# Kernel tuning notes

Measured on AMD Instinct MI355X. Metric: run time of the kernel, lower is better.

## Reference

```python
import jax, jax.numpy as jnp
import numpy as np
import math

B, S, D, NS, K, V = 4, 1024, 256, 64, 16, 32000
NEG = -10000.0


def l2n(x, axis=-1):
    # F.normalize with eps=1e-12
    return x / jnp.maximum(jnp.linalg.norm(x, axis=axis, keepdims=True), 1e-12)


def sparsemax(z, axis=-1):
    # sort descending, find support size k_z, threshold tau
    z_sorted = -jnp.sort(-z, axis=axis)
    cumsum = jnp.cumsum(z_sorted, axis=axis)
    n = z.shape[axis]
    k = jnp.arange(1, n + 1, dtype=z.dtype).reshape((1,) * (z.ndim - 1) + (n,))
    check = (1.0 + k * z_sorted > cumsum).astype(z.dtype)
    k_z = jnp.sum(check, axis=axis, keepdims=True)
    tau = (jnp.take_along_axis(cumsum, (k_z - 1).astype(jnp.int32), axis=axis) - 1.0) / k_z
    return jnp.maximum(z - tau, 0.0)


def router_forward(messages, hidden, x_ids, scn, mask, static_nb, geo_velocity,
                   ctx_conf, current_entropy, vel_proj_w, edge_w1, edge_b1,
                   edge_w2, edge_b2, probe_w, geo_gate_w, geo_gate_b):
    S_ = messages.shape[1]
    dg = jnp.eye(S_, dtype=bool)
    mfull = mask[None] | dg[None]  # masked_fill(mask) + diagonal fill combined

    # --- geodesic-endpoint routed attention ---
    endpoint = l2n(scn + 0.4 * geo_velocity)                      # [B,S,NS]
    endpoint_sim = jnp.einsum('bsn,btn->bst', endpoint, scn)      # [B,S,S]
    endpoint_sim = jnp.where(mfull, NEG, endpoint_sim)
    H_norm = jax.lax.stop_gradient(current_entropy)[..., None] / (math.log(V) + 1e-8)
    vel_h = geo_velocity @ vel_proj_w.T                           # [B,S,D]
    h_aimed = l2n(hidden + 0.3 * vel_h)
    h_msg_sim = jnp.einsum('bsd,btd->bst', h_aimed, messages)
    combined_geo = (endpoint_sim * H_norm + 0.5 * h_msg_sim) * 5.0
    combined_geo = jnp.where(mfull, NEG, combined_geo)
    ew_geo = sparsemax(combined_geo, axis=-1)
    geo_agg = jnp.einsum('bst,btd->bsd', ew_geo, messages)

    # --- vocab-neighbor match / aggregate ---
    nb_vocab = static_nb[x_ids]                                   # [B,S,K]
    match = (x_ids[:, None, None, :] == nb_vocab[..., None]).astype(messages.dtype)  # [B,S,K,S]
    causal = jnp.tril(jnp.ones((S_, S_), messages.dtype))
    match = match * causal[None, :, None, :]
    coverage = jnp.mean(jnp.minimum(jnp.sum(match, -1), 1.0), axis=-1, keepdims=True)  # [B,S,1]
    nb_msgs_s = jnp.einsum('bskp,bpd->bskd', match, messages)
    nb_scn_s = jnp.einsum('bskp,bpn->bskn', match, scn)
    sim_s = jnp.sum(nb_scn_s * scn[:, :, None, :], -1)            # [B,S,K]
    e = jax.nn.gelu(sim_s[..., None] @ edge_w1.T + edge_b1, approximate=False)
    e = (e @ edge_w2.T + edge_b2)[..., 0]
    ew_s = jax.nn.softmax(e, axis=-1)
    static_agg = jnp.sum(nb_msgs_s * ew_s[..., None], axis=2)     # [B,S,D]

    # --- local same-mode routing with sparsemax ---
    my_mode = jnp.argmax(scn, -1)
    same_mode = (my_mode[:, :, None] == my_mode[:, None, :]).astype(messages.dtype)
    same_mode = jnp.where(mfull, 0.0, same_mode)
    scn_sim = jnp.einsum('bsn,btn->bst', scn, scn) * same_mode
    has_nb = jnp.sum(same_mode, -1, keepdims=True) > 0
    pos = jnp.arange(S_, dtype=messages.dtype)
    pos_sim = -jnp.abs(pos[:, None] - pos[None, :])[None]
    pos_sim = jnp.where(mfull, NEG, pos_sim)
    routing_sim = jnp.where(has_nb, scn_sim, pos_sim * 0.01)
    routing_sim = jnp.where(mfull, NEG, routing_sim)
    ew_l = sparsemax(routing_sim * 5.0, axis=-1)
    local_agg = jnp.einsum('bst,btd->bsd', ew_l, messages)

    static_final = coverage * static_agg + (1.0 - coverage) * local_agg
    raw_gate = jax.nn.sigmoid(hidden @ geo_gate_w.T + geo_gate_b)
    geo_weight = raw_gate * ctx_conf
    agg = geo_weight * geo_agg + (1.0 - geo_weight) * static_final
    probe = l2n(hidden @ probe_w.T)
    agg_n = l2n(agg)
    rel = jax.nn.sigmoid(jnp.sum(agg_n * probe, -1, keepdims=True))
    return agg * rel


def setup_inputs() -> dict:
    key = jax.random.key(0)
    ks = jax.random.split(key, 14)
    messages = jax.random.normal(ks[0], (B, S, D), jnp.float32)
    hidden = jax.random.normal(ks[1], (B, S, D), jnp.float32)
    x_ids = jax.random.randint(ks[2], (B, S), 0, V)
    scn = jax.random.normal(ks[3], (B, S, NS), jnp.float32)
    mask = ~jnp.tril(jnp.ones((S, S), bool))  # True above diagonal (disallowed)
    static_nb = jax.random.randint(ks[4], (V, K), 0, V)
    geo_velocity = jax.random.normal(ks[5], (B, S, NS), jnp.float32) * 0.5
    ctx_conf = jax.random.uniform(ks[6], (B, S, 1), jnp.float32)
    current_entropy = jax.random.uniform(ks[7], (B, S), jnp.float32) * math.log(V)
    vel_proj_w = jax.random.normal(ks[8], (D, NS), jnp.float32) / np.sqrt(NS).astype(np.float32)
    edge_w1 = jax.random.normal(ks[9], (8, 1), jnp.float32)
    edge_b1 = jnp.zeros((8,), jnp.float32)
    edge_w2 = jax.random.normal(ks[10], (1, 8), jnp.float32) * 0.3
    edge_b2 = jnp.zeros((1,), jnp.float32)
    probe_w = jax.random.normal(ks[11], (D, D), jnp.float32) / np.sqrt(D).astype(np.float32)
    geo_gate_w = jax.random.normal(ks[12], (1, D), jnp.float32) * 0.02
    geo_gate_b = jnp.full((1,), -4.0, jnp.float32)
    return dict(messages=messages, hidden=hidden, x_ids=x_ids, scn=scn, mask=mask,
                static_nb=static_nb, geo_velocity=geo_velocity, ctx_conf=ctx_conf,
                current_entropy=current_entropy, vel_proj_w=vel_proj_w,
                edge_w1=edge_w1, edge_b1=edge_b1, edge_w2=edge_w2, edge_b2=edge_b2,
                probe_w=probe_w, geo_gate_w=geo_gate_w, geo_gate_b=geo_gate_b)


def reference(messages, hidden, x_ids, scn, mask, static_nb, geo_velocity, ctx_conf,
              current_entropy, vel_proj_w, edge_w1, edge_b1, edge_w2, edge_b2,
              probe_w, geo_gate_w, geo_gate_b):
    return router_forward(messages, hidden, x_ids, scn, mask, static_nb, geo_velocity,
                          ctx_conf, current_entropy, vel_proj_w, edge_w1, edge_b1,
                          edge_w2, edge_b2, probe_w, geo_gate_w, geo_gate_b)
```

## Files before the change

kernel.cpp:

```cpp
#include <hip/hip_runtime.h>
#include <math.h>

#define B_ 4
#define S_ 1024
#define D_ 256
#define NS_ 64
#define KNB 16
#define KPACK 320
#define NEG_ (-10000.0f)
#define LOGV_INV (1.0f/(10.373491181781864f + 1e-8f))
#define MCAP 64
#define NCHUNK 16
#define SUPCAP 1024

typedef __attribute__((ext_vector_type(8))) short short8;
typedef __attribute__((ext_vector_type(4))) float f32x4;


__device__ __forceinline__ void blockReduceSum4(float4& v, float* red) {
  #pragma unroll
  for (int off = 32; off > 0; off >>= 1) {
    v.x += __shfl_down(v.x, off, 64);
    v.y += __shfl_down(v.y, off, 64);
    v.z += __shfl_down(v.z, off, 64);
    v.w += __shfl_down(v.w, off, 64);
  }
  int lane = threadIdx.x & 63;
  int w = threadIdx.x >> 6;
  __syncthreads();
  if (lane == 0) {
    red[w] = v.x; red[4 + w] = v.y; red[8 + w] = v.z; red[12 + w] = v.w;
  }
  __syncthreads();
  v.x = red[0] + red[1] + red[2] + red[3];
  v.y = red[4] + red[5] + red[6] + red[7];
  v.z = red[8] + red[9] + red[10] + red[11];
  v.w = red[12] + red[13] + red[14] + red[15];
}

__device__ __forceinline__ void waveAllSum2(float& a, float& b) {
  #pragma unroll
  for (int off = 1; off < 64; off <<= 1) {
    a += __shfl_xor(a, off, 64);
    b += __shfl_xor(b, off, 64);
  }
}

__device__ __forceinline__ float michelot_tau16(const float* z) {
  float m = z[0];
  #pragma unroll
  for (int k = 1; k < 16; k++) m = fmaxf(m, z[k]);
  #pragma unroll
  for (int off = 1; off < 64; off <<= 1) m = fmaxf(m, __shfl_xor(m, off, 64));
  float thr = m - 1.0f;
  float s = 0.f, c = 0.f;
  #pragma unroll
  for (int k = 0; k < 16; k++) { float zk = z[k]; if (zk > thr) { s += zk; c += 1.f; } }
  waveAllSum2(s, c);
  int cnt = (int)c;
  float tau = (s - 1.0f) / c;
  for (int it = 0; it < 32; ++it) {
    float s2 = 0.f, c2 = 0.f;
    #pragma unroll
    for (int k = 0; k < 16; k++) { float zk = z[k]; if (zk > tau) { s2 += zk; c2 += 1.f; } }
    waveAllSum2(s2, c2);
    int ci = (int)c2;
    if (ci == cnt || ci == 0) break;
    cnt = ci;
    tau = (s2 - 1.0f) / c2;
  }
  return tau;
}

__device__ __forceinline__ unsigned short f2bf_rne(float f) {
  union { float f; unsigned u; } v; v.f = f;
  unsigned r = v.u + 0x7FFFu + ((v.u >> 16) & 1u);
  return (unsigned short)(r >> 16);
}
__device__ __forceinline__ float bf2f(unsigned short h) {
  union { unsigned u; float f; } v; v.u = ((unsigned)h) << 16;
  return v.f;
}
__device__ __forceinline__ void cvt_store4(unsigned short* hi, unsigned short* lo, float4 v) {
  unsigned short h0 = f2bf_rne(v.x), h1 = f2bf_rne(v.y), h2 = f2bf_rne(v.z), h3 = f2bf_rne(v.w);
  *(ushort4*)hi = make_ushort4(h0, h1, h2, h3);
  *(ushort4*)lo = make_ushort4(f2bf_rne(v.x - bf2f(h0)), f2bf_rne(v.y - bf2f(h1)),
                               f2bf_rne(v.z - bf2f(h2)), f2bf_rne(v.w - bf2f(h3)));
}
#define MFMA16(a,b,c) __builtin_amdgcn_mfma_f32_16x16x32_bf16((a),(b),(c),0,0,0)


__global__ __launch_bounds__(256) void msum_partial_kernel(
    const float* __restrict__ messages, float* __restrict__ part)
{
  int blk = blockIdx.x;
  int b = blk >> 4, c = blk & 15;
  int d = threadIdx.x;
  const float* src = messages + ((size_t)b * S_ + c * 64) * D_ + d;
  float acc = 0.f;
  #pragma unroll 8
  for (int t = 0; t < 64; t++) acc += src[t * D_];
  part[((size_t)b * NCHUNK + c) * D_ + d] = acc;
}


__global__ __launch_bounds__(256) void dual_gemm_kernel(
    const float* __restrict__ hidden, const float* __restrict__ gv,
    const float* __restrict__ probe_w, const float* __restrict__ vel_w,
    float* __restrict__ probe_raw, float* __restrict__ vel_h)
{
  __shared__ float As[32][68];
  __shared__ float Bs[32][68];
  int which = blockIdx.y;
  const float* A = which ? gv : hidden;
  const float* W = which ? vel_w : probe_w;
  float* C = which ? vel_h : probe_raw;
  int K = which ? NS_ : D_;

  int mt = blockIdx.x >> 2;
  int nt = blockIdx.x & 3;
  int s0 = mt * 64, t0 = nt * 64;

  int tid = threadIdx.x;
  int tx = tid & 15, ty = tid >> 4;
  float acc[4][4] = {{0.f}};

  for (int k0 = 0; k0 < K; k0 += 32) {
    #pragma unroll
    for (int l = 0; l < 2; l++) {
      int idx = tid + l * 256;
      int i = idx >> 3;
      int kf = idx & 7;
      float4 av = *(const float4*)(A + (size_t)(s0 + i) * K + k0 + kf*4);
      As[kf*4+0][i] = av.x; As[kf*4+1][i] = av.y; As[kf*4+2][i] = av.z; As[kf*4+3][i] = av.w;
      float4 bv = *(const float4*)(W + (size_t)(t0 + i) * K + k0 + kf*4);
      Bs[kf*4+0][i] = bv.x; Bs[kf*4+1][i] = bv.y; Bs[kf*4+2][i] = bv.z; Bs[kf*4+3][i] = bv.w;
    }
    __syncthreads();
    #pragma unroll
    for (int kk = 0; kk < 32; kk++) {
      float4 a4 = *(const float4*)&As[kk][ty*4];
      float4 b4 = *(const float4*)&Bs[kk][tx*4];
      float a[4] = {a4.x, a4.y, a4.z, a4.w};
      float bb[4] = {b4.x, b4.y, b4.z, b4.w};
      #pragma unroll
      for (int rr = 0; rr < 4; rr++)
        #pragma unroll
        for (int cc = 0; cc < 4; cc++)
          acc[rr][cc] += a[rr] * bb[cc];
    }
    __syncthreads();
  }

  #pragma unroll
  for (int rr = 0; rr < 4; rr++) {
    int srow = s0 + ty*4 + rr;
    float4 v = make_float4(acc[rr][0], acc[rr][1], acc[rr][2], acc[rr][3]);
    *(float4*)(C + (size_t)srow * D_ + t0 + tx*4) = v;
  }
}


__global__ __launch_bounds__(256) void prep2_kernel(
    const float* __restrict__ hidden,
    const float* __restrict__ scn, const float* __restrict__ gv,
    const float* __restrict__ ctx_conf, const float* __restrict__ entropy,
    const float* __restrict__ probe_raw, const float* __restrict__ vel_h,
    const float* __restrict__ gate_w, const float* __restrict__ gate_b,
    float* __restrict__ arow,
    float* __restrict__ probe, float* __restrict__ gw_out,
    int* __restrict__ mode_out)
{
  int r = blockIdx.x;
  int tid = threadIdx.x;
  __shared__ float sh_scn[NS_];
  __shared__ float red[16];

  float sv = 0.f, gvv = 0.f;
  if (tid < NS_) {
    sv  = scn[(size_t)r*NS_ + tid];
    gvv = gv[(size_t)r*NS_ + tid];
    sh_scn[tid] = sv;
  }
  float hid = hidden[(size_t)r*D_ + tid];
  float vh  = vel_h[(size_t)r*D_ + tid];
  float pr  = probe_raw[(size_t)r*D_ + tid];
  float gwt = gate_w[tid];

  float ep = (tid < NS_) ? (sv + 0.4f*gvv) : 0.f;
  float ha = hid + 0.3f*vh;

  float4 v = make_float4(ep*ep, ha*ha, pr*pr, hid*gwt);
  blockReduceSum4(v, red);

  float Hn = entropy[r] * LOGV_INV;
  float epn = fmaxf(sqrtf(v.x), 1e-12f);
  float han = fmaxf(sqrtf(v.y), 1e-12f);
  float prn = fmaxf(sqrtf(v.z), 1e-12f);

  if (tid < NS_) {
    arow[(size_t)r*KPACK + tid] = (5.0f*Hn) * (ep / epn);
  }
  arow[(size_t)r*KPACK + NS_ + tid] = 2.5f * (ha / han);
  probe[(size_t)r*D_ + tid] = pr / prn;

  if (tid == 0) {
    float rg = 1.f/(1.f + expf(-(v.w + gate_b[0])));
    gw_out[r] = rg * ctx_conf[r];
    float m = sh_scn[0]; int mi = 0;
    for (int n = 1; n < NS_; n++) { if (sh_scn[n] > m) { m = sh_scn[n]; mi = n; } }
    mode_out[r] = mi;
  }
}


#define GBT 64
#define GBK 32
#define NTRI 136
#define LDB 40

__global__ __launch_bounds__(256) void geo_gemm_mfma_kernel(
    const float* __restrict__ arow, const float* __restrict__ scn,
    const float* __restrict__ messages, float* __restrict__ z,
    float* __restrict__ sim)
{
  __shared__ unsigned short Ahi[GBT][LDB], Alo[GBT][LDB];
  __shared__ unsigned short Bhi[GBT][LDB], Blo[GBT][LDB];
  __shared__ unsigned short A2hi[GBT][LDB], A2lo[GBT][LDB];

  int blk = blockIdx.x;
  int b = blk / NTRI;
  int tri = blk % NTRI;
  int ts = 0;
  while ((ts + 1) * (ts + 2) / 2 <= tri) ts++;
  int tt = tri - ts * (ts + 1) / 2;
  int s0 = ts * GBT, t0 = tt * GBT;

  const float* A  = arow + (size_t)b * S_ * KPACK;
  const float* Bscn = scn + (size_t)b * S_ * NS_;
  const float* Bmsg = messages + (size_t)b * S_ * D_;

  int tid = threadIdx.x;
  int lane = tid & 63;
  int w = tid >> 6;
  int fm = lane & 15;
  int fq = lane >> 4;

  f32x4 accz[4], accs[4];
  #pragma unroll
  for (int i = 0; i < 4; i++) {
    accz[i] = (f32x4){0.f, 0.f, 0.f, 0.f};
    accs[i] = (f32x4){0.f, 0.f, 0.f, 0.f};
  }

  for (int k0 = 0; k0 < KPACK; k0 += GBK) {
    bool scn_slab = (k0 < NS_);
    #pragma unroll
    for (int l = 0; l < 2; l++) {
      int idx = tid + l * 256;
      int i = idx >> 3, kf = idx & 7;
      float4 av = *(const float4*)(A + (size_t)(s0 + i) * KPACK + k0 + kf*4);
      cvt_store4(&Ahi[i][kf*4], &Alo[i][kf*4], av);
      float4 bv;
      if (scn_slab) bv = *(const float4*)(Bscn + (size_t)(t0 + i) * NS_ + k0 + kf*4);
      else          bv = *(const float4*)(Bmsg + (size_t)(t0 + i) * D_ + (k0 - NS_) + kf*4);
      cvt_store4(&Bhi[i][kf*4], &Blo[i][kf*4], bv);
      if (scn_slab) {
        float4 cv = *(const float4*)(Bscn + (size_t)(s0 + i) * NS_ + k0 + kf*4);
        cvt_store4(&A2hi[i][kf*4], &A2lo[i][kf*4], cv);
      }
    }
    __syncthreads();

    short8 ah = *(const short8*)&Ahi[w*16 + fm][fq*8];
    short8 al = *(const short8*)&Alo[w*16 + fm][fq*8];
    short8 a2h, a2l;
    if (scn_slab) {
      a2h = *(const short8*)&A2hi[w*16 + fm][fq*8];
      a2l = *(const short8*)&A2lo[w*16 + fm][fq*8];
    }
    #pragma unroll
    for (int nt = 0; nt < 4; nt++) {
      short8 bh = *(const short8*)&Bhi[nt*16 + fm][fq*8];
      short8 bl = *(const short8*)&Blo[nt*16 + fm][fq*8];
      accz[nt] = MFMA16(ah, bh, accz[nt]);
      accz[nt] = MFMA16(ah, bl, accz[nt]);
      accz[nt] = MFMA16(al, bh, accz[nt]);
      if (scn_slab) {
        accs[nt] = MFMA16(a2h, bh, accs[nt]);
        accs[nt] = MFMA16(a2h, bl, accs[nt]);
        accs[nt] = MFMA16(a2l, bh, accs[nt]);
      }
    }
    __syncthreads();
  }

  float* zb = z + (size_t)b * S_ * S_;
  float* sb = sim + (size_t)b * S_ * S_;
  #pragma unroll
  for (int nt = 0; nt < 4; nt++) {
    #pragma unroll
    for (int rg = 0; rg < 4; rg++) {
      int row = s0 + w*16 + fq*4 + rg;
      int col = t0 + nt*16 + fm;
      zb[(size_t)row * S_ + col] = accz[nt][rg];
      sb[(size_t)row * S_ + col] = accs[nt][rg];
    }
  }
}


__global__ __launch_bounds__(256) void rows_fused7_kernel(
    const float* __restrict__ zbuf, const float* __restrict__ simbuf,
    const float* __restrict__ messages, const int* __restrict__ mode,
    const int* __restrict__ x_ids, const int* __restrict__ static_nb,
    const float* __restrict__ ew1, const float* __restrict__ eb1,
    const float* __restrict__ ew2, const float* __restrict__ eb2,
    const float* __restrict__ gw, const float* __restrict__ probe,
    const float* __restrict__ part, float* __restrict__ out)
{
  __shared__ int xb_l[S_];
  __shared__ int mode_l[S_];
  __shared__ float sim_lds[2][S_];
  __shared__ unsigned short gt_l[2][SUPCAP];
  __shared__ float gw_l[2][SUPCAP];
  __shared__ unsigned short lt_l[2][SUPCAP];
  __shared__ float lw_l[2][SUPCAP];
  __shared__ int gcnt_s[2], lcnt_s[2];
  __shared__ unsigned short mk_s[2][MCAP];
  __shared__ unsigned short mp_s[2][MCAP];
  __shared__ float ews[2][KNB];
  __shared__ float cov_s[2];
  __shared__ int M_s[2];
  __shared__ float red2[2][2][2];

  const int tid = threadIdx.x;
  const int lane = tid & 63;
  const int wv = tid >> 6;
  const int rw = wv >> 1;
  const int half = wv & 1;
  const int r = blockIdx.x * 2 + rw;
  const int b = r >> 10, s = r & 1023;
  const unsigned long long lmask_lt = (1ull << lane) - 1ull;

  const float2* msg2 = (const float2*)(messages + (size_t)b * S_ * D_);
  const int dbase = half * 64 + lane;

  ((int4*)xb_l)[tid]   = ((const int4*)(x_ids + (size_t)b * S_))[tid];
  ((int4*)mode_l)[tid] = ((const int4*)(mode + (size_t)b * S_))[tid];
  {
    int wr = tid & 127;
    const float4* simrow4 = (const float4*)(simbuf + (size_t)r * S_);
    if (wr * 4 <= s)         ((float4*)sim_lds[rw])[wr]       = simrow4[wr];
    if ((wr + 128) * 4 <= s) ((float4*)sim_lds[rw])[wr + 128] = simrow4[wr + 128];
  }
  __syncthreads();

  if (half == 0) {
    if (s != 0) {
      const float4* zrow4 = (const float4*)(zbuf + (size_t)r * S_);
      float zg[16];
      #pragma unroll
      for (int j = 0; j < 4; j++) {
        int t0 = j*256 + lane*4;
        if (j*256 < s) {
          float4 v = zrow4[j*64 + lane];
          zg[j*4+0] = (t0+0 < s) ? v.x : NEG_;
          zg[j*4+1] = (t0+1 < s) ? v.y : NEG_;
          zg[j*4+2] = (t0+2 < s) ? v.z : NEG_;
          zg[j*4+3] = (t0+3 < s) ? v.w : NEG_;
        } else {
          zg[j*4+0] = NEG_; zg[j*4+1] = NEG_; zg[j*4+2] = NEG_; zg[j*4+3] = NEG_;
        }
      }
      float tau = michelot_tau16(zg);
      int base = 0;
      #pragma unroll
      for (int k = 0; k < 16; k++) {
        float w = zg[k] - tau;
        bool p = w > 0.f;
        unsigned long long m = __ballot(p);
        if (p) {
          int idx = base + __popcll(m & lmask_lt);
          gt_l[rw][idx] = (unsigned short)((k >> 2)*256 + lane*4 + (k & 3));
          gw_l[rw][idx] = w;
        }
        base += __popcll(m);
      }
      if (lane == 0) gcnt_s[rw] = base;
    } else if (lane == 0) gcnt_s[rw] = 0;

    int xid = xb_l[s];
    int nb[KNB];
    #pragma unroll
    for (int k = 0; k < KNB; k++) nb[k] = static_nb[(size_t)xid * KNB + k];
    float simk[KNB];
    #pragma unroll
    for (int k = 0; k < KNB; k++) simk[k] = 0.f;
    unsigned int kmask = 0;
    int M = 0;
    for (int j = 0; j < 16; j++) {
      int p = j*64 + lane;
      int xp = xb_l[p];
      bool anym = false;
      #pragma unroll
      for (int k = 0; k < KNB; k++) anym |= (nb[k] == xp);
      anym = anym && (p <= s);
      unsigned long long m = __ballot(anym);
      while (m) {
        int ln = __ffsll((unsigned long long)m) - 1; m &= m - 1;
        int pp = j*64 + ln;
        int xpp = xb_l[pp];
        float d = sim_lds[rw][pp];
        #pragma unroll
        for (int k = 0; k < KNB; k++) {
          if (nb[k] == xpp) {
            if (M < MCAP && lane == 0) { mk_s[rw][M] = (unsigned short)k; mp_s[rw][M] = (unsigned short)pp; }
            M++;
            simk[k] += d;
            kmask |= (1u << k);
          }
        }
      }
    }
    if (M > MCAP) M = MCAP;
    if (lane == 0) { M_s[rw] = M; cov_s[rw] = (float)__popc(kmask) * (1.0f/(float)KNB); }
    if (M > 0) {
      if (lane == 0) {
        #pragma unroll
        for (int k = 0; k < KNB; k++) ews[rw][k] = simk[k];
      }
      float sim = (lane < KNB) ? ews[rw][lane] : 0.f;
      float e = eb2[0];
      #pragma unroll
      for (int j = 0; j < 8; j++) {
        float x = sim * ew1[j] + eb1[j];
        float gx = 0.5f * x * (1.0f + erff(x * 0.70710678118654752f));
        e += gx * ew2[j];
      }
      float mx = e;
      #pragma unroll
      for (int off = 1; off < 16; off <<= 1) mx = fmaxf(mx, __shfl_xor(mx, off, 64));
      float ex = expf(e - mx);
      float ssum = ex;
      #pragma unroll
      for (int off = 1; off < 16; off <<= 1) ssum += __shfl_xor(ssum, off, 64);
      if (lane < KNB) ews[rw][lane] = ex / ssum;
    }
  } else {
    if (s != 0) {
      int mode_s = mode_l[s];
      int cnt = 0;
      unsigned int pmask = 0;
      #pragma unroll
      for (int j = 0; j < 16; j++) {
        int t = j*64 + lane;
        bool p = (t < s) && (mode_l[t] == mode_s);
        if (p) pmask |= (1u << j);
        cnt += __popcll(__ballot(p));
      }
      bool has_nb = cnt > 0;
      float zl[16];
      #pragma unroll
      for (int j = 0; j < 16; j++) {
        int t = j*64 + lane;
        float zv;
        if (t >= s) zv = NEG_ * 5.0f;
        else if (pmask & (1u << j)) zv = sim_lds[rw][t] * 5.0f;
        else if (has_nb) zv = 0.f;
        else zv = (0.01f * (-(float)(s - t))) * 5.0f;
        zl[j] = zv;
      }
      float tau = michelot_tau16(zl);
      int base = 0;
      #pragma unroll
      for (int j = 0; j < 16; j++) {
        float w = zl[j] - tau;
        bool p = w > 0.f;
        unsigned long long m = __ballot(p);
        if (p) {
          int idx = base + __popcll(m & lmask_lt);
          lt_l[rw][idx] = (unsigned short)(j*64 + lane);
          lw_l[rw][idx] = w;
        }
        base += __popcll(m);
      }
      if (lane == 0) lcnt_s[rw] = base;
    } else if (lane == 0) lcnt_s[rw] = 0;
  }
  __syncthreads();

  float2 accg = {0.f, 0.f}, accl = {0.f, 0.f}, accs = {0.f, 0.f};
  if (s == 0) {
    const float2* part2 = (const float2*)(part + (size_t)b * NCHUNK * D_);
    float2 msum = {0.f, 0.f};
    #pragma unroll
    for (int c = 0; c < NCHUNK; c++) {
      float2 pm = part2[c * 128 + dbase];
      msum.x += pm.x; msum.y += pm.y;
    }
    accg.x = 0.0009765625f * msum.x; accg.y = 0.0009765625f * msum.y;
    accl.x = 0.00390625f * msum.x;   accl.y = 0.00390625f * msum.y;
  } else {
    int gc = gcnt_s[rw];
    for (int i = 0; i < gc; i++) {
      float w = gw_l[rw][i];
      float2 mm = msg2[(size_t)gt_l[rw][i] * 128 + dbase];
      accg.x += w*mm.x; accg.y += w*mm.y;
    }
    int lc = lcnt_s[rw];
    for (int i = 0; i < lc; i++) {
      float w = lw_l[rw][i];
      float2 mm = msg2[(size_t)lt_l[rw][i] * 128 + dbase];
      accl.x += w*mm.x; accl.y += w*mm.y;
    }
  }
  {
    int M = M_s[rw];
    for (int i = 0; i < M; i++) {
      int k = mk_s[rw][i], p = mp_s[rw][i];
      float w = ews[rw][k];
      float2 mm = msg2[(size_t)p * 128 + dbase];
      accs.x += w*mm.x; accs.y += w*mm.y;
    }
  }

  float g = gw[r];
  float cov = cov_s[rw];
  float2 agg;
  agg.x = g*accg.x + (1.f-g)*(cov*accs.x + (1.f-cov)*accl.x);
  agg.y = g*accg.y + (1.f-g)*(cov*accs.y + (1.f-cov)*accl.y);

  float2 pv = ((const float2*)probe)[(size_t)r * 128 + dbase];
  float n2 = agg.x*agg.x + agg.y*agg.y;
  float ap = agg.x*pv.x + agg.y*pv.y;
  waveAllSum2(n2, ap);
  if (lane == 0) { red2[rw][half][0] = n2; red2[rw][half][1] = ap; }
  __syncthreads();
  n2 = red2[rw][0][0] + red2[rw][1][0];
  ap = red2[rw][0][1] + red2[rw][1][1];
  float nrm = fmaxf(sqrtf(n2), 1e-12f);
  float rel = 1.f / (1.f + expf(-(ap / nrm)));
  float2 o;
  o.x = agg.x * rel; o.y = agg.y * rel;
  ((float2*)out)[(size_t)r * 128 + dbase] = o;
}


extern "C" void kernel_launch(void* const* d_in, const int* in_sizes, int n_in,
                              void* d_out, int out_size, void* d_ws, size_t ws_size,
                              hipStream_t stream)
{
  const float* messages  = (const float*)d_in[0];
  const float* hidden    = (const float*)d_in[1];
  const int*   x_ids     = (const int*)d_in[2];
  const float* scn       = (const float*)d_in[3];
  const int*   static_nb = (const int*)d_in[5];
  const float* gv        = (const float*)d_in[6];
  const float* ctx_conf  = (const float*)d_in[7];
  const float* entropy   = (const float*)d_in[8];
  const float* vel_w     = (const float*)d_in[9];
  const float* ew1       = (const float*)d_in[10];
  const float* eb1       = (const float*)d_in[11];
  const float* ew2       = (const float*)d_in[12];
  const float* eb2       = (const float*)d_in[13];
  const float* probe_w   = (const float*)d_in[14];
  const float* gate_w    = (const float*)d_in[15];
  const float* gate_b    = (const float*)d_in[16];
  float* out = (float*)d_out;

  float* ws      = (float*)d_ws;
  float* arow    = ws;
  float* probe   = arow    + (size_t)B_*S_*KPACK;
  float* gwbuf   = probe   + (size_t)B_*S_*D_;
  int*   mode    = (int*)(gwbuf + (size_t)B_*S_);
  float* zbuf    = (float*)(mode + (size_t)B_*S_);
  float* simbuf  = zbuf + (size_t)B_*S_*S_;
  float* vel_h   = simbuf + (size_t)B_*S_*S_;
  float* part    = vel_h + (size_t)B_*S_*D_;

  msum_partial_kernel<<<dim3(B_*NCHUNK), dim3(256), 0, stream>>>(messages, part);

  dual_gemm_kernel<<<dim3(256, 2), dim3(256), 0, stream>>>(
      hidden, gv, probe_w, vel_w, probe, vel_h);

  prep2_kernel<<<dim3(B_*S_), dim3(256), 0, stream>>>(
      hidden, scn, gv, ctx_conf, entropy, probe, vel_h,
      gate_w, gate_b, arow, probe, gwbuf, mode);

  geo_gemm_mfma_kernel<<<dim3(B_*NTRI), dim3(256), 0, stream>>>(
      arow, scn, messages, zbuf, simbuf);

  rows_fused7_kernel<<<dim3(B_*S_/2), dim3(256), 0, stream>>>(
      zbuf, simbuf, messages, mode, x_ids, static_nb,
      ew1, eb1, ew2, eb2, gwbuf, probe, part, out);
}
```

Baseline: 188.5 us.

## Pre-split inputs to bf16 hi/lo, use MFMA for dual GEMM, drop sim LDS staging

Adds a kernel that converts messages, hidden, scn, velocity and the weight matrices into bf16 hi/lo pairs once. The two small projection GEMMs then run on MFMA with a 3-term split instead of scalar FP32, and the geo GEMM loads pre-split bf16 tiles instead of converting inside every tile. The rows kernel stops staging the sim row in LDS and reads simbuf directly, using a shuffle for the match loop. This adds an extra pass and extra workspace traffic, and the hidden/gv splits alias zbuf before it is written.

```diff
diff --git a/kernel.cpp b/kernel.cpp
--- a/kernel.cpp
+++ b/kernel.cpp
@@ -14,6 +14,7 @@
 #define SUPCAP 1024
 
 typedef __attribute__((ext_vector_type(8))) short short8;
+typedef __attribute__((ext_vector_type(8))) unsigned short ushort8v;
 typedef __attribute__((ext_vector_type(4))) float f32x4;
 
 
@@ -88,6 +89,33 @@
                                f2bf_rne(v.z - bf2f(h2)), f2bf_rne(v.w - bf2f(h3)));
 }
 #define MFMA16(a,b,c) __builtin_amdgcn_mfma_f32_16x16x32_bf16((a),(b),(c),0,0,0)
+
+
+__global__ __launch_bounds__(256) void bf16_split_kernel(
+    const float* __restrict__ messages, const float* __restrict__ hidden,
+    const float* __restrict__ scn, const float* __restrict__ gv,
+    const float* __restrict__ probe_w, const float* __restrict__ vel_w,
+    unsigned short* __restrict__ msg_hi, unsigned short* __restrict__ msg_lo,
+    unsigned short* __restrict__ hid_hi, unsigned short* __restrict__ hid_lo,
+    unsigned short* __restrict__ scn_hi, unsigned short* __restrict__ scn_lo,
+    unsigned short* __restrict__ gv_hi,  unsigned short* __restrict__ gv_lo,
+    unsigned short* __restrict__ pw_hi,  unsigned short* __restrict__ pw_lo,
+    unsigned short* __restrict__ vw_hi,  unsigned short* __restrict__ vw_lo)
+{
+  const float* src; unsigned short *hi, *lo; int n;
+  switch (blockIdx.y) {
+    case 0: src = messages; hi = msg_hi; lo = msg_lo; n = B_*S_*D_;  break;
+    case 1: src = hidden;   hi = hid_hi; lo = hid_lo; n = B_*S_*D_;  break;
+    case 2: src = scn;      hi = scn_hi; lo = scn_lo; n = B_*S_*NS_; break;
+    case 3: src = gv;       hi = gv_hi;  lo = gv_lo;  n = B_*S_*NS_; break;
+    case 4: src = probe_w;  hi = pw_hi;  lo = pw_lo;  n = D_*D_;     break;
+    default: src = vel_w;   hi = vw_hi;  lo = vw_lo;  n = D_*NS_;    break;
+  }
+  int idx = (blockIdx.x * 256 + threadIdx.x) * 4;
+  if (idx >= n) return;
+  float4 v = *(const float4*)(src + idx);
+  cvt_store4(hi + idx, lo + idx, v);
+}
 
 
 __global__ __launch_bounds__(256) void msum_partial_kernel(
@@ -103,71 +131,70 @@
   part[((size_t)b * NCHUNK + c) * D_ + d] = acc;
 }
 
-
-__global__ __launch_bounds__(256) void dual_gemm_kernel(
-    const float* __restrict__ hidden, const float* __restrict__ gv,
-    const float* __restrict__ probe_w, const float* __restrict__ vel_w,
+#define LDB 40
+
+
+__global__ __launch_bounds__(256) void dual_gemm_mfma_kernel(
+    const unsigned short* __restrict__ hid_hi, const unsigned short* __restrict__ hid_lo,
+    const unsigned short* __restrict__ gv_hi,  const unsigned short* __restrict__ gv_lo,
+    const unsigned short* __restrict__ pw_hi,  const unsigned short* __restrict__ pw_lo,
+    const unsigned short* __restrict__ vw_hi,  const unsigned short* __restrict__ vw_lo,
     float* __restrict__ probe_raw, float* __restrict__ vel_h)
 {
-  __shared__ float As[32][68];
-  __shared__ float Bs[32][68];
+  __shared__ unsigned short Ahi[64][LDB], Alo[64][LDB];
+  __shared__ unsigned short Bhi[64][LDB], Blo[64][LDB];
   int which = blockIdx.y;
-  const float* A = which ? gv : hidden;
-  const float* W = which ? vel_w : probe_w;
+  const unsigned short* Ah = which ? gv_hi : hid_hi;
+  const unsigned short* Al = which ? gv_lo : hid_lo;
+  const unsigned short* Wh = which ? vw_hi : pw_hi;
+  const unsigned short* Wl = which ? vw_lo : pw_lo;
   float* C = which ? vel_h : probe_raw;
   int K = which ? NS_ : D_;
 
-  int mt = blockIdx.x >> 2;
-  int nt = blockIdx.x & 3;
-  int s0 = mt * 64, t0 = nt * 64;
-
-  int tid = threadIdx.x;
-  int tx = tid & 15, ty = tid >> 4;
-  float acc[4][4] = {{0.f}};
+  int mt = blockIdx.x >> 2, nt4 = blockIdx.x & 3;
+  int s0 = mt * 64, t0 = nt4 * 64;
+  int tid = threadIdx.x, lane = tid & 63, w = tid >> 6;
+  int fm = lane & 15, fq = lane >> 4;
+  int si = tid >> 2, sc = tid & 3;
+
+  f32x4 acc[4];
+  #pragma unroll
+  for (int i = 0; i < 4; i++) acc[i] = (f32x4){0.f, 0.f, 0.f, 0.f};
 
   for (int k0 = 0; k0 < K; k0 += 32) {
-    #pragma unroll
-    for (int l = 0; l < 2; l++) {
-      int idx = tid + l * 256;
-      int i = idx >> 3;
-      int kf = idx & 7;
-      float4 av = *(const float4*)(A + (size_t)(s0 + i) * K + k0 + kf*4);
-      As[kf*4+0][i] = av.x; As[kf*4+1][i] = av.y; As[kf*4+2][i] = av.z; As[kf*4+3][i] = av.w;
-      float4 bv = *(const float4*)(W + (size_t)(t0 + i) * K + k0 + kf*4);
-      Bs[kf*4+0][i] = bv.x; Bs[kf*4+1][i] = bv.y; Bs[kf*4+2][i] = bv.z; Bs[kf*4+3][i] = bv.w;
-    }
+    *(ushort8v*)&Ahi[si][sc*8] = *(const ushort8v*)(Ah + (size_t)(s0 + si) * K + k0 + sc*8);
+    *(ushort8v*)&Alo[si][sc*8] = *(const ushort8v*)(Al + (size_t)(s0 + si) * K + k0 + sc*8);
+    *(ushort8v*)&Bhi[si][sc*8] = *(const ushort8v*)(Wh + (size_t)(t0 + si) * K + k0 + sc*8);
+    *(ushort8v*)&Blo[si][sc*8] = *(const ushort8v*)(Wl + (size_t)(t0 + si) * K + k0 + sc*8);
     __syncthreads();
-    #pragma unroll
-    for (int kk = 0; kk < 32; kk++) {
-      float4 a4 = *(const float4*)&As[kk][ty*4];
-      float4 b4 = *(const float4*)&Bs[kk][tx*4];
-      float a[4] = {a4.x, a4.y, a4.z, a4.w};
-      float bb[4] = {b4.x, b4.y, b4.z, b4.w};
-      #pragma unroll
-      for (int rr = 0; rr < 4; rr++)
-        #pragma unroll
-        for (int cc = 0; cc < 4; cc++)
-          acc[rr][cc] += a[rr] * bb[cc];
+    short8 ah = *(const short8*)&Ahi[w*16 + fm][fq*8];
+    short8 al = *(const short8*)&Alo[w*16 + fm][fq*8];
+    #pragma unroll
+    for (int nt = 0; nt < 4; nt++) {
+      short8 bh = *(const short8*)&Bhi[nt*16 + fm][fq*8];
+      short8 bl = *(const short8*)&Blo[nt*16 + fm][fq*8];
+      acc[nt] = MFMA16(ah, bh, acc[nt]);
+      acc[nt] = MFMA16(ah, bl, acc[nt]);
+      acc[nt] = MFMA16(al, bh, acc[nt]);
     }
     __syncthreads();
   }
 
   #pragma unroll
-  for (int rr = 0; rr < 4; rr++) {
-    int srow = s0 + ty*4 + rr;
-    float4 v = make_float4(acc[rr][0], acc[rr][1], acc[rr][2], acc[rr][3]);
-    *(float4*)(C + (size_t)srow * D_ + t0 + tx*4) = v;
-  }
-}
-
-
-__global__ __launch_bounds__(256) void prep2_kernel(
+  for (int nt = 0; nt < 4; nt++)
+    #pragma unroll
+    for (int rg = 0; rg < 4; rg++)
+      C[(size_t)(s0 + w*16 + fq*4 + rg) * D_ + t0 + nt*16 + fm] = acc[nt][rg];
+}
+
+
+__global__ __launch_bounds__(256) void prep3_kernel(
     const float* __restrict__ hidden,
     const float* __restrict__ scn, const float* __restrict__ gv,
     const float* __restrict__ ctx_conf, const float* __restrict__ entropy,
     const float* __restrict__ probe_raw, const float* __restrict__ vel_h,
     const float* __restrict__ gate_w, const float* __restrict__ gate_b,
-    float* __restrict__ arow,
+    unsigned short* __restrict__ arow_hi, unsigned short* __restrict__ arow_lo,
     float* __restrict__ probe, float* __restrict__ gw_out,
     int* __restrict__ mode_out)
 {
@@ -199,9 +226,17 @@
   float prn = fmaxf(sqrtf(v.z), 1e-12f);
 
   if (tid < NS_) {
-    arow[(size_t)r*KPACK + tid] = (5.0f*Hn) * (ep / epn);
-  }
-  arow[(size_t)r*KPACK + NS_ + tid] = 2.5f * (ha / han);
+    float v0 = (5.0f*Hn) * (ep / epn);
+    unsigned short h = f2bf_rne(v0);
+    arow_hi[(size_t)r*KPACK + tid] = h;
+    arow_lo[(size_t)r*KPACK + tid] = f2bf_rne(v0 - bf2f(h));
+  }
+  {
+    float v1 = 2.5f * (ha / han);
+    unsigned short h = f2bf_rne(v1);
+    arow_hi[(size_t)r*KPACK + NS_ + tid] = h;
+    arow_lo[(size_t)r*KPACK + NS_ + tid] = f2bf_rne(v1 - bf2f(h));
+  }
   probe[(size_t)r*D_ + tid] = pr / prn;
 
   if (tid == 0) {
@@ -217,12 +252,12 @@
 #define GBT 64
 #define GBK 32
 #define NTRI 136
-#define LDB 40
-
-__global__ __launch_bounds__(256) void geo_gemm_mfma_kernel(
-    const float* __restrict__ arow, const float* __restrict__ scn,
-    const float* __restrict__ messages, float* __restrict__ z,
-    float* __restrict__ sim)
+
+__global__ __launch_bounds__(256) void geo_gemm_mfma2_kernel(
+    const unsigned short* __restrict__ arow_hi, const unsigned short* __restrict__ arow_lo,
+    const unsigned short* __restrict__ scn_hi,  const unsigned short* __restrict__ scn_lo,
+    const unsigned short* __restrict__ msg_hi,  const unsigned short* __restrict__ msg_lo,
+    float* __restrict__ z, float* __restrict__ sim)
 {
   __shared__ unsigned short Ahi[GBT][LDB], Alo[GBT][LDB];
   __shared__ unsigned short Bhi[GBT][LDB], Blo[GBT][LDB];
@@ -236,15 +271,16 @@
   int tt = tri - ts * (ts + 1) / 2;
   int s0 = ts * GBT, t0 = tt * GBT;
 
-  const float* A  = arow + (size_t)b * S_ * KPACK;
-  const float* Bscn = scn + (size_t)b * S_ * NS_;
-  const float* Bmsg = messages + (size_t)b * S_ * D_;
-
-  int tid = threadIdx.x;
-  int lane = tid & 63;
-  int w = tid >> 6;
-  int fm = lane & 15;
-  int fq = lane >> 4;
+  const unsigned short* Ah = arow_hi + (size_t)b * S_ * KPACK;
+  const unsigned short* Al = arow_lo + (size_t)b * S_ * KPACK;
+  const unsigned short* Sh = scn_hi + (size_t)b * S_ * NS_;
+  const unsigned short* Sl = scn_lo + (size_t)b * S_ * NS_;
+  const unsigned short* Mh = msg_hi + (size_t)b * S_ * D_;
+  const unsigned short* Ml = msg_lo + (size_t)b * S_ * D_;
+
+  int tid = threadIdx.x, lane = tid & 63, w = tid >> 6;
+  int fm = lane & 15, fq = lane >> 4;
+  int si = tid >> 2, sc = tid & 3;
 
   f32x4 accz[4], accs[4];
   #pragma unroll
@@ -255,20 +291,16 @@
 
   for (int k0 = 0; k0 < KPACK; k0 += GBK) {
     bool scn_slab = (k0 < NS_);
-    #pragma unroll
-    for (int l = 0; l < 2; l++) {
-      int idx = tid + l * 256;
-      int i = idx >> 3, kf = idx & 7;
-      float4 av = *(const float4*)(A + (size_t)(s0 + i) * KPACK + k0 + kf*4);
-      cvt_store4(&Ahi[i][kf*4], &Alo[i][kf*4], av);
-      float4 bv;
-      if (scn_slab) bv = *(const float4*)(Bscn + (size_t)(t0 + i) * NS_ + k0 + kf*4);
-      else          bv = *(const float4*)(Bmsg + (size_t)(t0 + i) * D_ + (k0 - NS_) + kf*4);
-      cvt_store4(&Bhi[i][kf*4], &Blo[i][kf*4], bv);
-      if (scn_slab) {
-        float4 cv = *(const float4*)(Bscn + (size_t)(s0 + i) * NS_ + k0 + kf*4);
-        cvt_store4(&A2hi[i][kf*4], &A2lo[i][kf*4], cv);
-      }
+    *(ushort8v*)&Ahi[si][sc*8] = *(const ushort8v*)(Ah + (size_t)(s0 + si) * KPACK + k0 + sc*8);
+    *(ushort8v*)&Alo[si][sc*8] = *(const ushort8v*)(Al + (size_t)(s0 + si) * KPACK + k0 + sc*8);
+    if (scn_slab) {
+      *(ushort8v*)&Bhi[si][sc*8]  = *(const ushort8v*)(Sh + (size_t)(t0 + si) * NS_ + k0 + sc*8);
+      *(ushort8v*)&Blo[si][sc*8]  = *(const ushort8v*)(Sl + (size_t)(t0 + si) * NS_ + k0 + sc*8);
+      *(ushort8v*)&A2hi[si][sc*8] = *(const ushort8v*)(Sh + (size_t)(s0 + si) * NS_ + k0 + sc*8);
+      *(ushort8v*)&A2lo[si][sc*8] = *(const ushort8v*)(Sl + (size_t)(s0 + si) * NS_ + k0 + sc*8);
+    } else {
+      *(ushort8v*)&Bhi[si][sc*8] = *(const ushort8v*)(Mh + (size_t)(t0 + si) * D_ + (k0 - NS_) + sc*8);
+      *(ushort8v*)&Blo[si][sc*8] = *(const ushort8v*)(Ml + (size_t)(t0 + si) * D_ + (k0 - NS_) + sc*8);
     }
     __syncthreads();
 
@@ -310,7 +342,7 @@
 }
 
 
-__global__ __launch_bounds__(256) void rows_fused7_kernel(
+__global__ __launch_bounds__(256) void rows_fused8_kernel(
     const float* __restrict__ zbuf, const float* __restrict__ simbuf,
     const float* __restrict__ messages, const int* __restrict__ mode,
     const int* __restrict__ x_ids, const int* __restrict__ static_nb,
@@ -321,7 +353,6 @@
 {
   __shared__ int xb_l[S_];
   __shared__ int mode_l[S_];
-  __shared__ float sim_lds[2][S_];
   __shared__ unsigned short gt_l[2][SUPCAP];
   __shared__ float gw_l[2][SUPCAP];
   __shared__ unsigned short lt_l[2][SUPCAP];
@@ -348,12 +379,6 @@
 
   ((int4*)xb_l)[tid]   = ((const int4*)(x_ids + (size_t)b * S_))[tid];
   ((int4*)mode_l)[tid] = ((const int4*)(mode + (size_t)b * S_))[tid];
-  {
-    int wr = tid & 127;
-    const float4* simrow4 = (const float4*)(simbuf + (size_t)r * S_);
-    if (wr * 4 <= s)         ((float4*)sim_lds[rw])[wr]       = simrow4[wr];
-    if ((wr + 128) * 4 <= s) ((float4*)sim_lds[rw])[wr + 128] = simrow4[wr + 128];
-  }
   __syncthreads();
 
   if (half == 0) {
@@ -406,12 +431,14 @@
       #pragma unroll
       for (int k = 0; k < KNB; k++) anym |= (nb[k] == xp);
       anym = anym && (p <= s);
+      float d_self = 0.f;
+      if (anym) d_self = simbuf[(size_t)r * S_ + p];
       unsigned long long m = __ballot(anym);
       while (m) {
         int ln = __ffsll((unsigned long long)m) - 1; m &= m - 1;
         int pp = j*64 + ln;
         int xpp = xb_l[pp];
-        float d = sim_lds[rw][pp];
+        float d = __shfl(d_self, ln, 64);
         #pragma unroll
         for (int k = 0; k < KNB; k++) {
           if (nb[k] == xpp) {
@@ -466,7 +493,7 @@
         int t = j*64 + lane;
         float zv;
         if (t >= s) zv = NEG_ * 5.0f;
-        else if (pmask & (1u << j)) zv = sim_lds[rw][t] * 5.0f;
+        else if (pmask & (1u << j)) zv = simbuf[(size_t)r * S_ + t] * 5.0f;
         else if (has_nb) zv = 0.f;
         else zv = (0.01f * (-(float)(s - t))) * 5.0f;
         zl[j] = zv;
@@ -569,29 +596,48 @@
   const float* gate_b    = (const float*)d_in[16];
   float* out = (float*)d_out;
 
-  float* ws      = (float*)d_ws;
-  float* arow    = ws;
-  float* probe   = arow    + (size_t)B_*S_*KPACK;
-  float* gwbuf   = probe   + (size_t)B_*S_*D_;
+  float* ws = (float*)d_ws;
+  float* probe   = ws;
+  float* gwbuf   = probe + (size_t)B_*S_*D_;
   int*   mode    = (int*)(gwbuf + (size_t)B_*S_);
   float* zbuf    = (float*)(mode + (size_t)B_*S_);
   float* simbuf  = zbuf + (size_t)B_*S_*S_;
   float* vel_h   = simbuf + (size_t)B_*S_*S_;
   float* part    = vel_h + (size_t)B_*S_*D_;
+  unsigned short* msg_hi  = (unsigned short*)(part + (size_t)B_*NCHUNK*D_);
+  unsigned short* msg_lo  = msg_hi  + (size_t)B_*S_*D_;
+  unsigned short* scn_hi  = msg_lo  + (size_t)B_*S_*D_;
+  unsigned short* scn_lo  = scn_hi  + (size_t)B_*S_*NS_;
+  unsigned short* arow_hi = scn_lo  + (size_t)B_*S_*NS_;
+  unsigned short* arow_lo = arow_hi + (size_t)B_*S_*KPACK;
+  unsigned short* hid_hi = (unsigned short*)zbuf;
+  unsigned short* hid_lo = hid_hi + (size_t)B_*S_*D_;
+  unsigned short* gv_hi  = hid_lo + (size_t)B_*S_*D_;
+  unsigned short* gv_lo  = gv_hi  + (size_t)B_*S_*NS_;
+  unsigned short* pw_hi  = gv_lo  + (size_t)B_*S_*NS_;
+  unsigned short* pw_lo  = pw_hi  + (size_t)D_*D_;
+  unsigned short* vw_hi  = pw_lo  + (size_t)D_*D_;
+  unsigned short* vw_lo  = vw_hi  + (size_t)D_*NS_;
+
+  bf16_split_kernel<<<dim3(1024, 6), dim3(256), 0, stream>>>(
+      messages, hidden, scn, gv, probe_w, vel_w,
+      msg_hi, msg_lo, hid_hi, hid_lo, scn_hi, scn_lo,
+      gv_hi, gv_lo, pw_hi, pw_lo, vw_hi, vw_lo);
 
   msum_partial_kernel<<<dim3(B_*NCHUNK), dim3(256), 0, stream>>>(messages, part);
 
-  dual_gemm_kernel<<<dim3(256, 2), dim3(256), 0, stream>>>(
-      hidden, gv, probe_w, vel_w, probe, vel_h);
-
-  prep2_kernel<<<dim3(B_*S_), dim3(256), 0, stream>>>(
+  dual_gemm_mfma_kernel<<<dim3(256, 2), dim3(256), 0, stream>>>(
+      hid_hi, hid_lo, gv_hi, gv_lo, pw_hi, pw_lo, vw_hi, vw_lo,
+      probe, vel_h);
+
+  prep3_kernel<<<dim3(B_*S_), dim3(256), 0, stream>>>(
       hidden, scn, gv, ctx_conf, entropy, probe, vel_h,
-      gate_w, gate_b, arow, probe, gwbuf, mode);
-
-  geo_gemm_mfma_kernel<<<dim3(B_*NTRI), dim3(256), 0, stream>>>(
-      arow, scn, messages, zbuf, simbuf);
-
-  rows_fused7_kernel<<<dim3(B_*S_/2), dim3(256), 0, stream>>>(
+      gate_w, gate_b, arow_hi, arow_lo, probe, gwbuf, mode);
+
+  geo_gemm_mfma2_kernel<<<dim3(B_*NTRI), dim3(256), 0, stream>>>(
+      arow_hi, arow_lo, scn_hi, scn_lo, msg_hi, msg_lo, zbuf, simbuf);
+
+  rows_fused8_kernel<<<dim3(B_*S_/2), dim3(256), 0, stream>>>(
       zbuf, simbuf, messages, mode, x_ids, static_nb,
       ew1, eb1, ew2, eb2, gwbuf, probe, part, out);
 }
```

Measured after the change: 180.2 us. 1.05x faster.
